# Optimization experiments

Hardware: AMD Instinct MI355X
Metric: run time of the kernel (lower is better)

The kernel has to match this reference:

```python
import jax, jax.numpy as jnp
import numpy as np

B, L, H, NH, HD, DI, NL = 8, 4096, 256, 4, 64, 1024, 6
_SCALE = 1.0 / np.sqrt(HD).astype(np.float32)


def _layernorm(x, g, b, eps=1e-5):
    m = x.mean(-1, keepdims=True)
    v = ((x - m) ** 2).mean(-1, keepdims=True)
    return (x - m) / jnp.sqrt(v + eps) * g + b


def _forward(data, mask, pos_emb, ln_g, ln_b, ff_w1, ff_b1, ff_w2, ff_b2,
             ff_lng, ff_lnb, ring_wq, ring_bq, ring_wk, ring_bk, ring_wv,
             ring_bv, ring_wo, ring_bo, star_wq, star_bq, star_wk, star_bk,
             star_wv, star_bv, star_wo, star_bo):
    pad = ~mask                                         # [B,L] True = padding
    spad = jnp.concatenate([jnp.zeros((B, 1), bool), pad], axis=1)  # [B,L+1]
    x = data + pos_emb[None, :L]                        # [B,L,H] (emb dropout = eval identity)
    nodes = x
    relay = x.mean(axis=1)                              # [B,H]
    for i in range(NL):
        # --- PositionwiseFeedForward (1x1 conv == dense over channels) ---
        h = nodes
        t = jax.nn.relu(h @ ff_w1[i].T + ff_b1[i]) @ ff_w2[i].T + ff_b2[i]
        h = _layernorm(t + h, ff_lng[i], ff_lnb[i])     # [B,L,H]
        # --- ring attention (_MSA1): size-3 sliding window + global relay key ---
        q = (h @ ring_wq[i].T + ring_bq[i]).reshape(B, L, NH, HD)
        k = (h @ ring_wk[i].T + ring_bk[i]).reshape(B, L, NH, HD)
        v = (h @ ring_wv[i].T + ring_bv[i]).reshape(B, L, NH, HD)
        kp = jnp.pad(k, ((0, 0), (1, 1), (0, 0), (0, 0)))  # zero pad, matches F.unfold
        vp = jnp.pad(v, ((0, 0), (1, 1), (0, 0), (0, 0)))
        k_win = jnp.stack([kp[:, 0:L], kp[:, 1:L + 1], kp[:, 2:L + 2]], axis=2)  # [B,L,3,NH,HD]
        v_win = jnp.stack([vp[:, 0:L], vp[:, 1:L + 1], vp[:, 2:L + 2]], axis=2)
        ak = (relay @ ring_wk[i].T + ring_bk[i]).reshape(B, 1, 1, NH, HD)
        av = (relay @ ring_wv[i].T + ring_bv[i]).reshape(B, 1, 1, NH, HD)
        k_all = jnp.concatenate([k_win, jnp.broadcast_to(ak, (B, L, 1, NH, HD))], axis=2)
        v_all = jnp.concatenate([v_win, jnp.broadcast_to(av, (B, L, 1, NH, HD))], axis=2)
        scores = jnp.einsum('blnd,blwnd->blwn', q, k_all) * _SCALE
        alphas = jax.nn.softmax(scores, axis=2)         # softmax over window dim (4)
        att = jnp.einsum('blwn,blwnd->blnd', alphas, v_all).reshape(B, L, NH * HD)
        ring_out = att @ ring_wo[i].T + ring_bo[i]
        nodes = jax.nn.leaky_relu(_layernorm(ring_out, ln_g[i], ln_b[i]))
        # --- star attention (_MSA2): relay attends to [relay; nodes] ---
        y = jnp.concatenate([relay[:, None, :], nodes], axis=1)  # [B,L+1,H]
        sq = (relay @ star_wq[i].T + star_bq[i]).reshape(B, NH, HD)
        sk = (y @ star_wk[i].T + star_bk[i]).reshape(B, L + 1, NH, HD)
        sv = (y @ star_wv[i].T + star_bv[i]).reshape(B, L + 1, NH, HD)
        s = jnp.einsum('bnd,blnd->bnl', sq, sk) * _SCALE
        s = jnp.where(spad[:, None, :], -jnp.inf, s)
        a = jax.nn.softmax(s, axis=-1)
        satt = jnp.einsum('bnl,blnd->bnd', a, sv).reshape(B, NH * HD)
        relay = jax.nn.leaky_relu(satt @ star_wo[i].T + star_bo[i])
        nodes = jnp.where(pad[:, :, None], 0.0, nodes)
    return nodes, relay


def setup_inputs() -> dict:
    key = jax.random.key(0)
    ks = iter(jax.random.split(key, 64))
    p = lambda shape: jax.random.normal(next(ks), shape, jnp.float32) * 0.02
    C = NH * HD
    return dict(
        data=jax.random.normal(next(ks), (B, L, H), jnp.float32),
        mask=jnp.ones((B, L), bool),
        pos_emb=p((L, H)),
        ln_g=jnp.ones((NL, H), jnp.float32), ln_b=jnp.zeros((NL, H), jnp.float32),
        ff_w1=p((NL, DI, H)), ff_b1=jnp.zeros((NL, DI), jnp.float32),
        ff_w2=p((NL, H, DI)), ff_b2=jnp.zeros((NL, H), jnp.float32),
        ff_lng=jnp.ones((NL, H), jnp.float32), ff_lnb=jnp.zeros((NL, H), jnp.float32),
        ring_wq=p((NL, C, H)), ring_bq=jnp.zeros((NL, C), jnp.float32),
        ring_wk=p((NL, C, H)), ring_bk=jnp.zeros((NL, C), jnp.float32),
        ring_wv=p((NL, C, H)), ring_bv=jnp.zeros((NL, C), jnp.float32),
        ring_wo=p((NL, H, C)), ring_bo=jnp.zeros((NL, H), jnp.float32),
        star_wq=p((NL, C, H)), star_bq=jnp.zeros((NL, C), jnp.float32),
        star_wk=p((NL, C, H)), star_bk=jnp.zeros((NL, C), jnp.float32),
        star_wv=p((NL, C, H)), star_bv=jnp.zeros((NL, C), jnp.float32),
        star_wo=p((NL, H, C)), star_bo=jnp.zeros((NL, H), jnp.float32),
    )


def reference(data, mask, pos_emb, ln_g, ln_b, ff_w1, ff_b1, ff_w2, ff_b2,
              ff_lng, ff_lnb, ring_wq, ring_bq, ring_wk, ring_bk, ring_wv,
              ring_bv, ring_wo, ring_bo, star_wq, star_bq, star_wk, star_bk,
              star_wv, star_bv, star_wo, star_bo):
    return _forward(data, mask, pos_emb, ln_g, ln_b, ff_w1, ff_b1, ff_w2,
                    ff_b2, ff_lng, ff_lnb, ring_wq, ring_bq, ring_wk, ring_bk,
                    ring_wv, ring_bv, ring_wo, ring_bo, star_wq, star_bq,
                    star_wk, star_bk, star_wv, star_bv, star_wo, star_bo)
```

## Files before the change

### kernel.cpp

```cpp
#include <hip/hip_runtime.h>
#include <hip/hip_bf16.h>

#define B_ 8
#define L_ 4096
#define H_ 256
#define NH_ 4
#define DI_ 1024
#define NL_ 6
#define TOK_ (B_*L_)

typedef unsigned short u16;
typedef __attribute__((ext_vector_type(8))) short short8;
typedef __attribute__((ext_vector_type(4))) float f32x4;

struct __align__(8) u16x4 { u16 x,y,z,w; };

__device__ __forceinline__ float bf2f(u16 u){
  union { unsigned u; float f; } c; c.u = ((unsigned)u)<<16; return c.f;
}
__device__ __forceinline__ u16 f2bf(float f){
  union { float f; unsigned u; } c; c.f = f;
  unsigned r = c.u + 0x7FFF + ((c.u>>16)&1);
  return (u16)(r>>16);
}
__device__ __forceinline__ void gload_lds16(const short* g, short* l){
  __builtin_amdgcn_global_load_lds(
      (const __attribute__((address_space(1))) void*)g,
      (__attribute__((address_space(3))) void*)l, 16, 0, 0);
}
__device__ __forceinline__ void block_sync(){
  asm volatile("" ::: "memory");
  __builtin_amdgcn_s_barrier();
  __builtin_amdgcn_sched_barrier(0);
}
#define WAIT_VMCNT(N) asm volatile("s_waitcnt vmcnt(" #N ")" ::: "memory")

template<bool RELU, bool OBF16>
__global__ __launch_bounds__(512, 4) void gemm_bt(
    const u16* __restrict__ A, const u16* __restrict__ W,
    const float* __restrict__ bias, void* __restrict__ out, int N, int K, int nbn)
{
  constexpr int BM=128, BK=64;
  __shared__ __align__(16) short As[2][BM*BK];
  __shared__ __align__(16) short Ws[2][BM*BK];
  const int tid = threadIdx.x, lane = tid&63, wid = tid>>6;
  const int wm = wid>>1, wn = wid&1;
  const int id = blockIdx.x;
  const int xcd = id & 7, j = id >> 3;
  const int bm = xcd*32 + j / nbn;
  const int bn = j % nbn;
  const short* Ag = (const short*)A + (size_t)bm*BM*K;
  const short* Wg = (const short*)W + (size_t)bn*BM*K;
  f32x4 acc[2][4] = {};

  auto STAGE = [&](int k0, int buf){
    #pragma unroll
    for (int jj=0;jj<2;++jj){
      int c = jj*512 + tid;
      int row = c>>3;
      int col = (c&7) ^ (row&7);
      const size_t src = (size_t)row*K + k0 + col*8;
      gload_lds16(Ag + src, &As[buf][(size_t)c*8]);
      gload_lds16(Wg + src, &Ws[buf][(size_t)c*8]);
    }
  };
  auto COMPUTE = [&](int cur){
    #pragma unroll
    for (int kk=0;kk<BK;kk+=32){
      short8 af[2], bfr[4];
      int kc = (kk>>3) + (lane>>4);
      #pragma unroll
      for (int ms=0;ms<2;++ms){
        int r = wm*32 + ms*16 + (lane&15);
        af[ms] = *(const short8*)&As[cur][r*BK + ((kc ^ (r&7))<<3)];
      }
      #pragma unroll
      for (int ns=0;ns<4;++ns){
        int r = wn*64 + ns*16 + (lane&15);
        bfr[ns] = *(const short8*)&Ws[cur][r*BK + ((kc ^ (r&7))<<3)];
      }
      #pragma unroll
      for (int ms=0;ms<2;++ms)
        #pragma unroll
        for (int ns=0;ns<4;++ns)
          acc[ms][ns] = __builtin_amdgcn_mfma_f32_16x16x32_bf16(af[ms], bfr[ns], acc[ms][ns], 0, 0, 0);
    }
  };

  const int NT = K/BK;
  STAGE(0, 0); STAGE(BK, 1);
  WAIT_VMCNT(4);
  block_sync();
  for (int t=0;t<NT;++t){
    const int cur = t&1;
    __builtin_amdgcn_s_setprio(1);
    COMPUTE(cur);
    __builtin_amdgcn_s_setprio(0);
    block_sync();
    if (t+2 < NT) STAGE((t+2)*BK, cur);
    if (t+1 < NT){
      if (t+2 < NT) { WAIT_VMCNT(4); }
      else          { WAIT_VMCNT(0); }
      block_sync();
    }
  }
  if (OBF16){
    constexpr int OP = 136;
    u16* O = (u16*)&As[0][0];
    #pragma unroll
    for (int ns=0;ns<4;++ns){
      int lc = wn*64 + ns*16 + (lane&15);
      float bc = bias[bn*BM + lc];
      #pragma unroll
      for (int ms=0;ms<2;++ms){
        int rbase = wm*32 + ms*16 + ((lane>>4)<<2);
        #pragma unroll
        for (int i=0;i<4;++i){
          float v = acc[ms][ns][i] + bc;
          if (RELU) v = fmaxf(v, 0.f);
          O[(rbase+i)*OP + lc] = f2bf(v);
        }
      }
    }
    block_sync();
    u16* ob = (u16*)out + (size_t)bm*BM*N + bn*BM;
    const int rr = tid>>4;
    const int cc = (tid&15)<<3;
    #pragma unroll
    for (int p=0;p<4;++p){
      int r = p*32 + rr;
      *reinterpret_cast<short8*>(ob + (size_t)r*N + cc) =
          *reinterpret_cast<const short8*>(&O[r*OP + cc]);
    }
  } else {
    const int r0 = bm*BM + wm*32;
    const int c0 = bn*BM + wn*64;
    #pragma unroll
    for (int ns=0;ns<4;++ns){
      int col = c0 + ns*16 + (lane&15);
      float bc = bias[col];
      #pragma unroll
      for (int ms=0;ms<2;++ms){
        int rbase = r0 + ms*16 + ((lane>>4)<<2);
        #pragma unroll
        for (int i=0;i<4;++i){
          float v = acc[ms][ns][i] + bc;
          if (RELU) v = fmaxf(v, 0.f);
          ((float*)out)[(size_t)(rbase+i)*N + col] = v;
        }
      }
    }
  }
}

template<bool ADDRES, bool LEAKY>
__global__ __launch_bounds__(512, 4) void gemm_ln(
    const u16* __restrict__ A, const u16* __restrict__ W,
    const float* __restrict__ bias, const u16* __restrict__ res,
    const float* __restrict__ g, const float* __restrict__ bv,
    u16* __restrict__ outb, float* __restrict__ outf, int K)
{
  constexpr int BM=64, BK=64;
  __shared__ __align__(16) short As[2][BM*BK];
  __shared__ __align__(16) short Ws[2][256*BK];
  float* S1  = (float*)&As[0][0];
  float* S2  = S1 + 64*4;
  float* MU  = S2 + 64*4;
  float* RSD = MU + 64;
  const int tid = threadIdx.x, lane = tid&63, wid = tid>>6;
  const int wm = wid>>2, wn = wid&3;
  const int m0 = blockIdx.x*BM;
  const short* Ag = (const short*)A + (size_t)m0*K;
  const short* Wg = (const short*)W;
  f32x4 acc[2][4] = {};

  auto STAGE = [&](int k0, int buf){
    {
      int c = tid;
      int row = c>>3;
      int col = (c&7) ^ (row&7);
      gload_lds16(Ag + (size_t)row*K + k0 + col*8, &As[buf][(size_t)c*8]);
    }
    #pragma unroll
    for (int jj=0;jj<4;++jj){
      int c = jj*512 + tid;
      int row = c>>3;
      int col = (c&7) ^ (row&7);
      gload_lds16(Wg + (size_t)row*K + k0 + col*8, &Ws[buf][(size_t)c*8]);
    }
  };
  auto COMPUTE = [&](int cur){
    #pragma unroll
    for (int kk=0;kk<BK;kk+=32){
      short8 af[2], bfr[4];
      int kc = (kk>>3) + (lane>>4);
      #pragma unroll
      for (int ms=0;ms<2;++ms){
        int r = wm*32 + ms*16 + (lane&15);
        af[ms] = *(const short8*)&As[cur][r*BK + ((kc ^ (r&7))<<3)];
      }
      #pragma unroll
      for (int ns=0;ns<4;++ns){
        int r = wn*64 + ns*16 + (lane&15);
        bfr[ns] = *(const short8*)&Ws[cur][r*BK + ((kc ^ (r&7))<<3)];
      }
      #pragma unroll
      for (int ms=0;ms<2;++ms)
        #pragma unroll
        for (int ns=0;ns<4;++ns)
          acc[ms][ns] = __builtin_amdgcn_mfma_f32_16x16x32_bf16(af[ms], bfr[ns], acc[ms][ns], 0, 0, 0);
    }
  };

  const int NT = K/BK;
  STAGE(0, 0); STAGE(BK, 1);
  WAIT_VMCNT(5);
  block_sync();
  for (int t=0;t<NT;++t){
    const int cur = t&1;
    __builtin_amdgcn_s_setprio(1);
    COMPUTE(cur);
    __builtin_amdgcn_s_setprio(0);
    block_sync();
    if (t+2 < NT) STAGE((t+2)*BK, cur);
    if (t+1 < NT){
      if (t+2 < NT) { WAIT_VMCNT(5); }
      else          { WAIT_VMCNT(0); }
      block_sync();
    }
  }
  #pragma unroll
  for (int ns=0;ns<4;++ns){
    int col = wn*64 + ns*16 + (lane&15);
    float bc = bias[col];
    #pragma unroll
    for (int ms=0;ms<2;++ms){
      int rl = wm*32 + ms*16 + ((lane>>4)<<2);
      #pragma unroll
      for (int i=0;i<4;++i){
        float v = acc[ms][ns][i] + bc;
        if (ADDRES) v += bf2f(res[(size_t)(m0+rl+i)*256 + col]);
        acc[ms][ns][i] = v;
      }
    }
  }
  #pragma unroll
  for (int ms=0;ms<2;++ms)
    #pragma unroll
    for (int i=0;i<4;++i){
      float p1 = acc[ms][0][i]+acc[ms][1][i]+acc[ms][2][i]+acc[ms][3][i];
      float p2 = acc[ms][0][i]*acc[ms][0][i] + acc[ms][1][i]*acc[ms][1][i]
               + acc[ms][2][i]*acc[ms][2][i] + acc[ms][3][i]*acc[ms][3][i];
      #pragma unroll
      for (int o=1;o<16;o<<=1){ p1 += __shfl_xor(p1,o,64); p2 += __shfl_xor(p2,o,64); }
      if ((lane&15)==0){
        int rl = wm*32 + ms*16 + ((lane>>4)<<2) + i;
        S1[rl*4 + wn] = p1; S2[rl*4 + wn] = p2;
      }
    }
  __syncthreads();
  if (tid < 64){
    float s1 = S1[tid*4+0]+S1[tid*4+1]+S1[tid*4+2]+S1[tid*4+3];
    float s2 = S2[tid*4+0]+S2[tid*4+1]+S2[tid*4+2]+S2[tid*4+3];
    float mean = s1*(1.f/256.f);
    float var = fmaxf(s2*(1.f/256.f) - mean*mean, 0.f);
    MU[tid] = mean; RSD[tid] = 1.f/sqrtf(var + 1e-5f);
  }
  __syncthreads();
  constexpr int OP = 268;
  u16* O = (u16*)&Ws[0][0];
  #pragma unroll
  for (int ns=0;ns<4;++ns){
    int col = wn*64 + ns*16 + (lane&15);
    float gg = g[col], bb = bv[col];
    #pragma unroll
    for (int ms=0;ms<2;++ms){
      int rl = wm*32 + ms*16 + ((lane>>4)<<2);
      #pragma unroll
      for (int i=0;i<4;++i){
        float y = (acc[ms][ns][i] - MU[rl+i])*RSD[rl+i]*gg + bb;
        if (LEAKY) y = y>0.f ? y : 0.01f*y;
        O[(rl+i)*OP + col] = f2bf(y);
        if (outf) outf[(size_t)(m0+rl+i)*256 + col] = y;
      }
    }
  }
  __syncthreads();
  u16* ob = outb + (size_t)m0*256;
  const int rr = tid>>5;
  const int cc = (tid&31)<<3;
  #pragma unroll
  for (int p=0;p<4;++p){
    int r = p*16 + rr;
    *reinterpret_cast<short8*>(ob + ((size_t)r<<8) + cc) =
        *reinterpret_cast<const short8*>(&O[r*OP + cc]);
  }
}

__global__ __launch_bounds__(256) void ring_attn(
    const u16* __restrict__ qkv, const float* __restrict__ akav, u16* __restrict__ att)
{
  const int g = blockIdx.x*4 + (threadIdx.x>>6);
  const int lane = threadIdx.x & 63;
  const int l = g & (L_-1);
  const int b = g >> 12;
  const size_t tok = (size_t)g;
  float q[4], kp[4], kc[4], kn[4], ak[4], vp[4], vc[4], vn[4], av[4];
  {
    u16x4 t = *(const u16x4*)(qkv + tok*768 + lane*4);
    q[0]=bf2f(t.x); q[1]=bf2f(t.y); q[2]=bf2f(t.z); q[3]=bf2f(t.w);
    t = *(const u16x4*)(qkv + tok*768 + 256 + lane*4);
    kc[0]=bf2f(t.x); kc[1]=bf2f(t.y); kc[2]=bf2f(t.z); kc[3]=bf2f(t.w);
    t = *(const u16x4*)(qkv + tok*768 + 512 + lane*4);
    vc[0]=bf2f(t.x); vc[1]=bf2f(t.y); vc[2]=bf2f(t.z); vc[3]=bf2f(t.w);
    if (l>0){
      t = *(const u16x4*)(qkv + (tok-1)*768 + 256 + lane*4);
      kp[0]=bf2f(t.x); kp[1]=bf2f(t.y); kp[2]=bf2f(t.z); kp[3]=bf2f(t.w);
      t = *(const u16x4*)(qkv + (tok-1)*768 + 512 + lane*4);
      vp[0]=bf2f(t.x); vp[1]=bf2f(t.y); vp[2]=bf2f(t.z); vp[3]=bf2f(t.w);
    } else { kp[0]=kp[1]=kp[2]=kp[3]=0.f; vp[0]=vp[1]=vp[2]=vp[3]=0.f; }
    if (l<L_-1){
      t = *(const u16x4*)(qkv + (tok+1)*768 + 256 + lane*4);
      kn[0]=bf2f(t.x); kn[1]=bf2f(t.y); kn[2]=bf2f(t.z); kn[3]=bf2f(t.w);
      t = *(const u16x4*)(qkv + (tok+1)*768 + 512 + lane*4);
      vn[0]=bf2f(t.x); vn[1]=bf2f(t.y); vn[2]=bf2f(t.z); vn[3]=bf2f(t.w);
    } else { kn[0]=kn[1]=kn[2]=kn[3]=0.f; vn[0]=vn[1]=vn[2]=vn[3]=0.f; }
    float4 f = ((const float4*)(akav + (size_t)b*H_))[lane];
    ak[0]=f.x; ak[1]=f.y; ak[2]=f.z; ak[3]=f.w;
    f = ((const float4*)(akav + 2048 + (size_t)b*H_))[lane];
    av[0]=f.x; av[1]=f.y; av[2]=f.z; av[3]=f.w;
  }
  float dp=0.f, dc=0.f, dn=0.f, da=0.f;
  #pragma unroll
  for (int j=0;j<4;++j){ dp += q[j]*kp[j]; dc += q[j]*kc[j]; dn += q[j]*kn[j]; da += q[j]*ak[j]; }
  #pragma unroll
  for (int o=1;o<16;o<<=1){
    dp += __shfl_xor(dp,o,64); dc += __shfl_xor(dc,o,64);
    dn += __shfl_xor(dn,o,64); da += __shfl_xor(da,o,64);
  }
  dp *= 0.125f; dc *= 0.125f; dn *= 0.125f; da *= 0.125f;
  float m = fmaxf(fmaxf(dp,dc), fmaxf(dn,da));
  float e0 = expf(dp-m), e1 = expf(dc-m), e2 = expf(dn-m), e3 = expf(da-m);
  float rd = 1.f/(e0+e1+e2+e3);
  u16x4 o4;
  o4.x = f2bf((e0*vp[0]+e1*vc[0]+e2*vn[0]+e3*av[0])*rd);
  o4.y = f2bf((e0*vp[1]+e1*vc[1]+e2*vn[1]+e3*av[1])*rd);
  o4.z = f2bf((e0*vp[2]+e1*vc[2]+e2*vn[2]+e3*av[2])*rd);
  o4.w = f2bf((e0*vp[3]+e1*vc[3]+e2*vn[3]+e3*av[3])*rd);
  *(u16x4*)(att + tok*H_ + lane*4) = o4;
}

__global__ __launch_bounds__(256) void star_scores(
    const u16* __restrict__ skv, const float* __restrict__ sq,
    const float* __restrict__ sk0, float* __restrict__ s)
{
  const int g = blockIdx.x*4 + (threadIdx.x>>6);
  if (g >= B_*(L_+1)) return;
  const int lane = threadIdx.x & 63;
  const int b = g/(L_+1), j = g%(L_+1);
  float4 qv = ((const float4*)(sq + (size_t)b*H_))[lane];
  float k0,k1,k2,k3;
  if (j==0){
    float4 kv = ((const float4*)(sk0 + (size_t)b*H_))[lane];
    k0=kv.x; k1=kv.y; k2=kv.z; k3=kv.w;
  } else {
    u16x4 t = *(const u16x4*)(skv + ((size_t)b*L_ + (j-1))*512 + lane*4);
    k0=bf2f(t.x); k1=bf2f(t.y); k2=bf2f(t.z); k3=bf2f(t.w);
  }
  float d = qv.x*k0 + qv.y*k1 + qv.z*k2 + qv.w*k3;
  #pragma unroll
  for (int o=1;o<16;o<<=1) d += __shfl_xor(d,o,64);
  if ((lane&15)==0)
    s[(size_t)(b*4 + (lane>>4))*(L_+1) + j] = d*0.125f;
}

__global__ __launch_bounds__(1024) void star_softmax(float* __restrict__ s)
{
  const int bh = blockIdx.x;
  float* row = s + (size_t)bh*(L_+1);
  __shared__ float red[1024];
  const int tid = threadIdx.x;
  float m = -1e30f;
  for (int j=tid; j<L_+1; j+=1024) m = fmaxf(m, row[j]);
  red[tid] = m; __syncthreads();
  for (int st=512; st>0; st>>=1){ if (tid<st) red[tid] = fmaxf(red[tid], red[tid+st]); __syncthreads(); }
  m = red[0]; __syncthreads();
  float sum = 0.f;
  for (int j=tid; j<L_+1; j+=1024){ float e = expf(row[j]-m); row[j] = e; sum += e; }
  red[tid] = sum; __syncthreads();
  for (int st=512; st>0; st>>=1){ if (tid<st) red[tid] += red[tid+st]; __syncthreads(); }
  const float rs = 1.f/red[0];
  for (int j=tid; j<L_+1; j+=1024) row[j] *= rs;
}

__global__ __launch_bounds__(256) void star_satt_part(
    const float* __restrict__ a, const u16* __restrict__ skv, float* __restrict__ part)
{
  const int blk = blockIdx.x;
  const int b = blk >> 6, seg = blk & 63;
  const int tid = threadIdx.x, q4 = tid & 63, sub = tid >> 6;
  const int h = q4 >> 4;
  const float* arow = a + (size_t)(b*4 + h)*(L_+1) + 1;
  float a0=0.f,a1=0.f,a2=0.f,a3=0.f;
  const int j0 = seg*64 + sub*16;
  #pragma unroll 4
  for (int jj=j0; jj<j0+16; ++jj){
    u16x4 v = *(const u16x4*)(skv + ((size_t)b*L_ + jj)*512 + 256 + q4*4);
    float al = arow[jj];
    a0 += al*bf2f(v.x); a1 += al*bf2f(v.y); a2 += al*bf2f(v.z); a3 += al*bf2f(v.w);
  }
  __shared__ float red[4][256];
  red[sub][q4*4+0]=a0; red[sub][q4*4+1]=a1; red[sub][q4*4+2]=a2; red[sub][q4*4+3]=a3;
  __syncthreads();
  if (sub==0){
    #pragma unroll
    for (int c=0;c<4;++c){
      int ch = q4*4+c;
      part[(size_t)blk*256 + ch] = red[0][ch]+red[1][ch]+red[2][ch]+red[3][ch];
    }
  }
}

__global__ __launch_bounds__(256) void pack_wT(
    const float* __restrict__ w0, const float* __restrict__ w1,
    const float* __restrict__ w2, const float* __restrict__ w3,
    const float* __restrict__ w4, const float* __restrict__ w5,
    float* __restrict__ T)
{
  __shared__ float tile[32][33];
  const int blk = blockIdx.x;
  const int t = blk & 63, m = blk >> 6;
  const int l = m / 6, w = m % 6;
  const float* srcs[6] = {w0, w1, w2, w3, w4, w5};
  const float* src = srcs[w] + (size_t)l*65536;
  const int r0 = (t>>3)*32, c0 = (t&7)*32;
  const int rr = threadIdx.x >> 5, cc = threadIdx.x & 31;
  #pragma unroll
  for (int p=0;p<4;++p)
    tile[rr + p*8][cc] = src[(size_t)(r0 + rr + p*8)*256 + c0 + cc];
  __syncthreads();
  float* dst = T + (size_t)m*65536;
  #pragma unroll
  for (int p=0;p<4;++p)
    dst[(size_t)(c0 + rr + p*8)*256 + r0 + cc] = tile[cc][rr + p*8];
}

struct TPB { const float* b; float* out; };
struct TPB5 { TPB p[5]; };
__global__ __launch_bounds__(256) void relay_projs(
    const float* __restrict__ relay, const float* __restrict__ TW, TPB5 tp)
{
  const int b = blockIdx.x, w = blockIdx.y, n = threadIdx.x;
  __shared__ float rs[H_];
  rs[n] = relay[b*H_ + n];
  __syncthreads();
  const float* wt = TW + (size_t)w*65536;
  float s = tp.p[w].b[n];
  #pragma unroll 8
  for (int c=0;c<H_;++c) s += rs[c]*wt[(size_t)c*256 + n];
  tp.p[w].out[b*H_+n] = s;
}

__global__ __launch_bounds__(256) void relay_tail_k(
    const float* __restrict__ part, const float* __restrict__ a,
    const float* __restrict__ sv0, const float* __restrict__ TW,
    const float* __restrict__ bo, float* __restrict__ relay, float* __restrict__ outr)
{
  const int b = blockIdx.x, n = threadIdx.x;
  __shared__ float rs[H_];
  const int h = n >> 6;
  float s = a[(size_t)(b*4+h)*(L_+1)] * sv0[b*H_ + n];
  #pragma unroll 8
  for (int g2=0; g2<64; ++g2) s += part[((size_t)b*64+g2)*256 + n];
  rs[n] = s;
  __syncthreads();
  const float* wt = TW + (size_t)5*65536;
  float v = bo[n];
  #pragma unroll 8
  for (int c=0;c<H_;++c) v += rs[c]*wt[(size_t)c*256 + n];
  v = v>0.f ? v : 0.01f*v;
  relay[b*H_+n] = v;
  if (outr) outr[b*H_+n] = v;
}

__global__ void f32_to_bf16_k(const float* __restrict__ s, u16* __restrict__ d, int n){
  for (int i = blockIdx.x*blockDim.x + threadIdx.x; i < n; i += gridDim.x*blockDim.x)
    d[i] = f2bf(s[i]);
}
__global__ void pack_wqkv(const float* __restrict__ wq, const float* __restrict__ wk,
                          const float* __restrict__ wv, u16* __restrict__ dst){
  const int n = NL_*768*H_;
  for (int i = blockIdx.x*blockDim.x + threadIdx.x; i < n; i += gridDim.x*blockDim.x){
    int l = i/(768*H_); int rem = i%(768*H_); int r = rem/H_; int c = rem%H_;
    float v = (r<256) ? wq[((size_t)l*H_ + r)*H_ + c]
            : (r<512) ? wk[((size_t)l*H_ + (r-256))*H_ + c]
                      : wv[((size_t)l*H_ + (r-512))*H_ + c];
    dst[i] = f2bf(v);
  }
}
__global__ void pack_wskv(const float* __restrict__ wk, const float* __restrict__ wv, u16* __restrict__ dst){
  const int n = NL_*512*H_;
  for (int i = blockIdx.x*blockDim.x + threadIdx.x; i < n; i += gridDim.x*blockDim.x){
    int l = i/(512*H_); int rem = i%(512*H_); int r = rem/H_; int c = rem%H_;
    float v = (r<256) ? wk[((size_t)l*H_ + r)*H_ + c]
                      : wv[((size_t)l*H_ + (r-256))*H_ + c];
    dst[i] = f2bf(v);
  }
}
__global__ void pack_biases(const float* __restrict__ bq, const float* __restrict__ bk,
                            const float* __restrict__ bv, float* __restrict__ dqkv,
                            const float* __restrict__ sbk, const float* __restrict__ sbv,
                            float* __restrict__ dskv){
  int i = blockIdx.x*blockDim.x + threadIdx.x;
  if (i < NL_*768){
    int l = i/768, r = i%768;
    dqkv[i] = (r<256) ? bq[l*H_+r] : (r<512) ? bk[l*H_+r-256] : bv[l*H_+r-512];
  }
  if (i < NL_*512){
    int l = i/512, r = i%512;
    dskv[i] = (r<256) ? sbk[l*H_+r] : sbv[l*H_+r-256];
  }
}
__global__ void init_nodes(const float* __restrict__ data, const float* __restrict__ pos, u16* __restrict__ nodes){
  const int total = TOK_*H_/4;
  int i = blockIdx.x*blockDim.x + threadIdx.x;
  if (i >= total) return;
  float4 d = ((const float4*)data)[i];
  float4 p = ((const float4*)pos)[i % (L_*H_/4)];
  u16x4 o; o.x=f2bf(d.x+p.x); o.y=f2bf(d.y+p.y); o.z=f2bf(d.z+p.z); o.w=f2bf(d.w+p.w);
  ((u16x4*)nodes)[i] = o;
}
__global__ void relay_partial(const float* __restrict__ data, const float* __restrict__ pos, float* __restrict__ part){
  const int b = blockIdx.x>>3, seg = blockIdx.x&7, hh = threadIdx.x;
  float s = 0.f;
  for (int l = seg*512; l < seg*512+512; ++l)
    s += data[((size_t)b*L_ + l)*H_ + hh] + pos[(size_t)l*H_ + hh];
  part[blockIdx.x*H_ + hh] = s;
}
__global__ void relay_combine(const float* __restrict__ part, float* __restrict__ relay){
  const int b = blockIdx.x, hh = threadIdx.x;
  float s = 0.f;
  for (int g=0; g<8; ++g) s += part[(b*8+g)*H_ + hh];
  relay[b*H_+hh] = s * (1.0f/L_);
}

extern "C" void kernel_launch(void* const* d_in, const int* in_sizes, int n_in,
                              void* d_out, int out_size, void* d_ws, size_t ws_size,
                              hipStream_t stream)
{
  const float* data   = (const float*)d_in[0];
  const float* pos    = (const float*)d_in[2];
  const float* ln_g   = (const float*)d_in[3];
  const float* ln_b   = (const float*)d_in[4];
  const float* ff_w1  = (const float*)d_in[5];
  const float* ff_b1  = (const float*)d_in[6];
  const float* ff_w2  = (const float*)d_in[7];
  const float* ff_b2  = (const float*)d_in[8];
  const float* ff_lng = (const float*)d_in[9];
  const float* ff_lnb = (const float*)d_in[10];
  const float* ring_wq= (const float*)d_in[11]; const float* ring_bq= (const float*)d_in[12];
  const float* ring_wk= (const float*)d_in[13]; const float* ring_bk= (const float*)d_in[14];
  const float* ring_wv= (const float*)d_in[15]; const float* ring_bv= (const float*)d_in[16];
  const float* ring_wo= (const float*)d_in[17]; const float* ring_bo= (const float*)d_in[18];
  const float* star_wq= (const float*)d_in[19]; const float* star_bq= (const float*)d_in[20];
  const float* star_wk= (const float*)d_in[21]; const float* star_bk= (const float*)d_in[22];
  const float* star_wv= (const float*)d_in[23]; const float* star_bv= (const float*)d_in[24];
  const float* star_wo= (const float*)d_in[25]; const float* star_bo= (const float*)d_in[26];

  char* ws = (char*)d_ws;
  size_t off = 0;
  auto alc = [&](size_t n){ size_t cur = off; off = (cur + n + 255) & ~(size_t)255; return (void*)(ws + cur); };
  u16*  W1B   = (u16*)alc((size_t)NL_*DI_*H_*2);
  u16*  W2B   = (u16*)alc((size_t)NL_*H_*DI_*2);
  u16*  WQKVB = (u16*)alc((size_t)NL_*768*H_*2);
  u16*  WOB   = (u16*)alc((size_t)NL_*H_*H_*2);
  u16*  WSKVB = (u16*)alc((size_t)NL_*512*H_*2);
  float* BQKVB= (float*)alc((size_t)NL_*768*4);
  float* BSKVB= (float*)alc((size_t)NL_*512*4);
  float* TWB  = (float*)alc((size_t)NL_*6*H_*H_*4);
  u16*  NB    = (u16*)alc((size_t)TOK_*H_*2);
  u16*  HB    = (u16*)alc((size_t)TOK_*H_*2);
  u16*  T1R   = (u16*)alc((size_t)TOK_*DI_*2);
  float* RELAY  = (float*)alc(B_*H_*4);
  float* PART   = (float*)alc(64*H_*4);
  float* AKAV   = (float*)alc(2*B_*H_*4);
  float* SQB    = (float*)alc(B_*H_*4);
  float* SK0B   = (float*)alc(B_*H_*4);
  float* SV0B   = (float*)alc(B_*H_*4);
  float* SBUF   = (float*)alc((size_t)B_*NH_*(L_+1)*4);
  float* SPART  = (float*)alc((size_t)B_*64*256*4);
  u16* QKVB = T1R;
  u16* ATTB = T1R + (size_t)TOK_*768;
  u16* SKVB = T1R;

  f32_to_bf16_k<<<2048, 256, 0, stream>>>(ff_w1, W1B, NL_*DI_*H_);
  f32_to_bf16_k<<<2048, 256, 0, stream>>>(ff_w2, W2B, NL_*H_*DI_);
  f32_to_bf16_k<<<1024, 256, 0, stream>>>(ring_wo, WOB, NL_*H_*H_);
  pack_wqkv<<<2048, 256, 0, stream>>>(ring_wq, ring_wk, ring_wv, WQKVB);
  pack_wskv<<<2048, 256, 0, stream>>>(star_wk, star_wv, WSKVB);
  pack_biases<<<18, 256, 0, stream>>>(ring_bq, ring_bk, ring_bv, BQKVB, star_bk, star_bv, BSKVB);
  pack_wT<<<NL_*6*64, 256, 0, stream>>>(ring_wk, ring_wv, star_wq, star_wk, star_wv, star_wo, TWB);

  init_nodes<<<(TOK_*H_/4 + 255)/256, 256, 0, stream>>>(data, pos, NB);
  relay_partial<<<64, 256, 0, stream>>>(data, pos, PART);
  relay_combine<<<B_, 256, 0, stream>>>(PART, RELAY);

  for (int l=0; l<NL_; ++l){
    const float* TWl = TWB + (size_t)l*6*H_*H_;
    gemm_bt<true,true><<<(DI_/128)*(TOK_/128), 512, 0, stream>>>(
        NB, W1B + (size_t)l*DI_*H_, ff_b1 + l*DI_, T1R, DI_, H_, DI_/128);
    gemm_ln<true,false><<<TOK_/64, 512, 0, stream>>>(
        T1R, W2B + (size_t)l*H_*DI_, ff_b2 + l*H_, NB,
        ff_lng + l*H_, ff_lnb + l*H_, HB, nullptr, DI_);
    TPB5 tp;
    tp.p[0] = { ring_bk + l*H_, AKAV };
    tp.p[1] = { ring_bv + l*H_, AKAV + 2048 };
    tp.p[2] = { star_bq + l*H_, SQB };
    tp.p[3] = { star_bk + l*H_, SK0B };
    tp.p[4] = { star_bv + l*H_, SV0B };
    relay_projs<<<dim3(B_,5), 256, 0, stream>>>(RELAY, TWl, tp);
    gemm_bt<false,true><<<(768/128)*(TOK_/128), 512, 0, stream>>>(
        HB, WQKVB + (size_t)l*768*H_, BQKVB + l*768, QKVB, 768, H_, 768/128);
    ring_attn<<<TOK_/4, 256, 0, stream>>>(QKVB, AKAV, ATTB);
    gemm_ln<false,true><<<TOK_/64, 512, 0, stream>>>(
        ATTB, WOB + (size_t)l*H_*H_, ring_bo + l*H_, nullptr,
        ln_g + l*H_, ln_b + l*H_, NB,
        (l==NL_-1) ? (float*)d_out : nullptr, H_);
    gemm_bt<false,true><<<(512/128)*(TOK_/128), 512, 0, stream>>>(
        NB, WSKVB + (size_t)l*512*H_, BSKVB + l*512, SKVB, 512, H_, 512/128);
    star_scores<<<(B_*(L_+1) + 3)/4, 256, 0, stream>>>(SKVB, SQB, SK0B, SBUF);
    star_softmax<<<B_*NH_, 1024, 0, stream>>>(SBUF);
    star_satt_part<<<B_*64, 256, 0, stream>>>(SBUF, SKVB, SPART);
    relay_tail_k<<<B_, 256, 0, stream>>>(SPART, SBUF, SV0B, TWl,
        star_bo + l*H_, RELAY,
        (l==NL_-1) ? ((float*)d_out + (size_t)TOK_*H_) : nullptr);
  }
}
```

Measured before the change: 1.097 ms.

## Fuse ring attention into output-projection GEMM with LayerNorm epilogue

Replaces the separate ring_attn kernel and the following gemm_ln with a single attn_ln kernel. Each 64-row block computes the windowed attention output directly into a swizzled LDS A tile, then runs the Wo GEMM while streaming W in double-buffered chunks, and applies bias, LayerNorm and leaky ReLU in the epilogue. This removes one launch and the global write and re-read of the attention tensor. In exchange it uses much more LDS per block, which may lower occupancy, and the attention loads are serialised ahead of the GEMM.

Measured after the change: 1.072 ms. 1.02x faster.

```diff
diff --git a/kernel.cpp b/kernel.cpp
--- a/kernel.cpp
+++ b/kernel.cpp
@@ -34,6 +34,7 @@
   __builtin_amdgcn_sched_barrier(0);
 }
 #define WAIT_VMCNT(N) asm volatile("s_waitcnt vmcnt(" #N ")" ::: "memory")
+#define WAIT_LGKM0()  asm volatile("s_waitcnt lgkmcnt(0)" ::: "memory")
 
 template<bool RELU, bool OBF16>
 __global__ __launch_bounds__(512, 4) void gemm_bt(
@@ -297,57 +298,186 @@
   }
 }
 
-__global__ __launch_bounds__(256) void ring_attn(
-    const u16* __restrict__ qkv, const float* __restrict__ akav, u16* __restrict__ att)
-{
-  const int g = blockIdx.x*4 + (threadIdx.x>>6);
-  const int lane = threadIdx.x & 63;
-  const int l = g & (L_-1);
-  const int b = g >> 12;
-  const size_t tok = (size_t)g;
-  float q[4], kp[4], kc[4], kn[4], ak[4], vp[4], vc[4], vn[4], av[4];
-  {
-    u16x4 t = *(const u16x4*)(qkv + tok*768 + lane*4);
-    q[0]=bf2f(t.x); q[1]=bf2f(t.y); q[2]=bf2f(t.z); q[3]=bf2f(t.w);
-    t = *(const u16x4*)(qkv + tok*768 + 256 + lane*4);
-    kc[0]=bf2f(t.x); kc[1]=bf2f(t.y); kc[2]=bf2f(t.z); kc[3]=bf2f(t.w);
-    t = *(const u16x4*)(qkv + tok*768 + 512 + lane*4);
-    vc[0]=bf2f(t.x); vc[1]=bf2f(t.y); vc[2]=bf2f(t.z); vc[3]=bf2f(t.w);
+__global__ __launch_bounds__(512, 4) void attn_ln(
+    const u16* __restrict__ qkv, const float* __restrict__ akav,
+    const u16* __restrict__ W, const float* __restrict__ bo,
+    const float* __restrict__ g, const float* __restrict__ bv,
+    u16* __restrict__ outb, float* __restrict__ outf)
+{
+  constexpr int BK=32, NT=256/BK;
+  __shared__ __align__(16) char LB[74240];
+  short* Afull = (short*)LB;
+  short* Ws2   = (short*)(LB + 32768);
+  float* S1  = (float*)(LB + 65536);
+  float* S2  = S1 + 256;
+  float* MU  = S2 + 256;
+  float* RSD = MU + 64;
+  const int tid = threadIdx.x, lane = tid&63, wid = tid>>6;
+  const int wm = wid>>2, wn = wid&3;
+  const int m0 = blockIdx.x*64;
+  const short* Wg = (const short*)W;
+
+  auto STAGE_W = [&](int k0, int buf){
+    #pragma unroll
+    for (int jj=0;jj<2;++jj){
+      int c = jj*512 + tid;
+      int row = c>>2;
+      int col = (c&3) ^ (row&3);
+      gload_lds16(Wg + (size_t)row*256 + k0 + col*8, &Ws2[(size_t)buf*8192 + (size_t)c*8]);
+    }
+  };
+
+  STAGE_W(0, 0); STAGE_W(BK, 1);
+  __builtin_amdgcn_sched_barrier(0);
+
+  for (int it=0; it<8; ++it){
+    const int rl = wid*8 + it;
+    const size_t tok = (size_t)(m0 + rl);
+    const int l = (int)(tok & (L_-1));
+    const int b = (int)(tok >> 12);
+    float q[4], kp[4], kc[4], kn[4], ak[4], vp[4], vc[4], vn[4], av[4];
+    u16x4 t4 = *(const u16x4*)(qkv + tok*768 + lane*4);
+    q[0]=bf2f(t4.x); q[1]=bf2f(t4.y); q[2]=bf2f(t4.z); q[3]=bf2f(t4.w);
+    t4 = *(const u16x4*)(qkv + tok*768 + 256 + lane*4);
+    kc[0]=bf2f(t4.x); kc[1]=bf2f(t4.y); kc[2]=bf2f(t4.z); kc[3]=bf2f(t4.w);
+    t4 = *(const u16x4*)(qkv + tok*768 + 512 + lane*4);
+    vc[0]=bf2f(t4.x); vc[1]=bf2f(t4.y); vc[2]=bf2f(t4.z); vc[3]=bf2f(t4.w);
     if (l>0){
-      t = *(const u16x4*)(qkv + (tok-1)*768 + 256 + lane*4);
-      kp[0]=bf2f(t.x); kp[1]=bf2f(t.y); kp[2]=bf2f(t.z); kp[3]=bf2f(t.w);
-      t = *(const u16x4*)(qkv + (tok-1)*768 + 512 + lane*4);
-      vp[0]=bf2f(t.x); vp[1]=bf2f(t.y); vp[2]=bf2f(t.z); vp[3]=bf2f(t.w);
+      t4 = *(const u16x4*)(qkv + (tok-1)*768 + 256 + lane*4);
+      kp[0]=bf2f(t4.x); kp[1]=bf2f(t4.y); kp[2]=bf2f(t4.z); kp[3]=bf2f(t4.w);
+      t4 = *(const u16x4*)(qkv + (tok-1)*768 + 512 + lane*4);
+      vp[0]=bf2f(t4.x); vp[1]=bf2f(t4.y); vp[2]=bf2f(t4.z); vp[3]=bf2f(t4.w);
     } else { kp[0]=kp[1]=kp[2]=kp[3]=0.f; vp[0]=vp[1]=vp[2]=vp[3]=0.f; }
     if (l<L_-1){
-      t = *(const u16x4*)(qkv + (tok+1)*768 + 256 + lane*4);
-      kn[0]=bf2f(t.x); kn[1]=bf2f(t.y); kn[2]=bf2f(t.z); kn[3]=bf2f(t.w);
-      t = *(const u16x4*)(qkv + (tok+1)*768 + 512 + lane*4);
-      vn[0]=bf2f(t.x); vn[1]=bf2f(t.y); vn[2]=bf2f(t.z); vn[3]=bf2f(t.w);
+      t4 = *(const u16x4*)(qkv + (tok+1)*768 + 256 + lane*4);
+      kn[0]=bf2f(t4.x); kn[1]=bf2f(t4.y); kn[2]=bf2f(t4.z); kn[3]=bf2f(t4.w);
+      t4 = *(const u16x4*)(qkv + (tok+1)*768 + 512 + lane*4);
+      vn[0]=bf2f(t4.x); vn[1]=bf2f(t4.y); vn[2]=bf2f(t4.z); vn[3]=bf2f(t4.w);
     } else { kn[0]=kn[1]=kn[2]=kn[3]=0.f; vn[0]=vn[1]=vn[2]=vn[3]=0.f; }
-    float4 f = ((const float4*)(akav + (size_t)b*H_))[lane];
-    ak[0]=f.x; ak[1]=f.y; ak[2]=f.z; ak[3]=f.w;
-    f = ((const float4*)(akav + 2048 + (size_t)b*H_))[lane];
-    av[0]=f.x; av[1]=f.y; av[2]=f.z; av[3]=f.w;
-  }
-  float dp=0.f, dc=0.f, dn=0.f, da=0.f;
-  #pragma unroll
-  for (int j=0;j<4;++j){ dp += q[j]*kp[j]; dc += q[j]*kc[j]; dn += q[j]*kn[j]; da += q[j]*ak[j]; }
-  #pragma unroll
-  for (int o=1;o<16;o<<=1){
-    dp += __shfl_xor(dp,o,64); dc += __shfl_xor(dc,o,64);
-    dn += __shfl_xor(dn,o,64); da += __shfl_xor(da,o,64);
-  }
-  dp *= 0.125f; dc *= 0.125f; dn *= 0.125f; da *= 0.125f;
-  float m = fmaxf(fmaxf(dp,dc), fmaxf(dn,da));
-  float e0 = expf(dp-m), e1 = expf(dc-m), e2 = expf(dn-m), e3 = expf(da-m);
-  float rd = 1.f/(e0+e1+e2+e3);
-  u16x4 o4;
-  o4.x = f2bf((e0*vp[0]+e1*vc[0]+e2*vn[0]+e3*av[0])*rd);
-  o4.y = f2bf((e0*vp[1]+e1*vc[1]+e2*vn[1]+e3*av[1])*rd);
-  o4.z = f2bf((e0*vp[2]+e1*vc[2]+e2*vn[2]+e3*av[2])*rd);
-  o4.w = f2bf((e0*vp[3]+e1*vc[3]+e2*vn[3]+e3*av[3])*rd);
-  *(u16x4*)(att + tok*H_ + lane*4) = o4;
+    float4 f4 = ((const float4*)(akav + (size_t)b*H_))[lane];
+    ak[0]=f4.x; ak[1]=f4.y; ak[2]=f4.z; ak[3]=f4.w;
+    f4 = ((const float4*)(akav + 2048 + (size_t)b*H_))[lane];
+    av[0]=f4.x; av[1]=f4.y; av[2]=f4.z; av[3]=f4.w;
+    float dp=0.f, dc=0.f, dn=0.f, da=0.f;
+    #pragma unroll
+    for (int jc=0;jc<4;++jc){ dp += q[jc]*kp[jc]; dc += q[jc]*kc[jc]; dn += q[jc]*kn[jc]; da += q[jc]*ak[jc]; }
+    #pragma unroll
+    for (int o=1;o<16;o<<=1){
+      dp += __shfl_xor(dp,o,64); dc += __shfl_xor(dc,o,64);
+      dn += __shfl_xor(dn,o,64); da += __shfl_xor(da,o,64);
+    }
+    dp *= 0.125f; dc *= 0.125f; dn *= 0.125f; da *= 0.125f;
+    float m = fmaxf(fmaxf(dp,dc), fmaxf(dn,da));
+    float e0 = expf(dp-m), e1 = expf(dc-m), e2 = expf(dn-m), e3 = expf(da-m);
+    float rd = 1.f/(e0+e1+e2+e3);
+    u16x4 o4;
+    o4.x = f2bf((e0*vp[0]+e1*vc[0]+e2*vn[0]+e3*av[0])*rd);
+    o4.y = f2bf((e0*vp[1]+e1*vc[1]+e2*vn[1]+e3*av[1])*rd);
+    o4.z = f2bf((e0*vp[2]+e1*vc[2]+e2*vn[2]+e3*av[2])*rd);
+    o4.w = f2bf((e0*vp[3]+e1*vc[3]+e2*vn[3]+e3*av[3])*rd);
+    int gq = lane>>1;
+    int s = (gq & ~7) | ((gq&7) ^ (rl&7));
+    *(u16x4*)&Afull[rl*256 + s*8 + (lane&1)*4] = o4;
+  }
+  WAIT_LGKM0();
+  WAIT_VMCNT(2);
+  block_sync();
+
+  f32x4 acc[2][4] = {};
+  for (int t=0;t<NT;++t){
+    const int cur = t&1;
+    __builtin_amdgcn_s_setprio(1);
+    {
+      short8 af[2], bfr[4];
+      #pragma unroll
+      for (int ms=0;ms<2;++ms){
+        int r = wm*32 + ms*16 + (lane&15);
+        int gk = t*4 + (lane>>4);
+        int s = (gk & ~7) | ((gk&7) ^ (r&7));
+        af[ms] = *(const short8*)&Afull[r*256 + s*8];
+      }
+      #pragma unroll
+      for (int ns=0;ns<4;++ns){
+        int r2 = wn*64 + ns*16 + (lane&15);
+        int sl = (lane>>4) ^ (r2&3);
+        bfr[ns] = *(const short8*)&Ws2[(size_t)cur*8192 + r2*32 + sl*8];
+      }
+      #pragma unroll
+      for (int ms=0;ms<2;++ms)
+        #pragma unroll
+        for (int ns=0;ns<4;++ns)
+          acc[ms][ns] = __builtin_amdgcn_mfma_f32_16x16x32_bf16(af[ms], bfr[ns], acc[ms][ns], 0, 0, 0);
+    }
+    __builtin_amdgcn_s_setprio(0);
+    block_sync();
+    if (t+2 < NT) STAGE_W((t+2)*BK, cur);
+    if (t+1 < NT){
+      if (t+2 < NT) { WAIT_VMCNT(2); }
+      else          { WAIT_VMCNT(0); }
+      block_sync();
+    }
+  }
+
+  #pragma unroll
+  for (int ns=0;ns<4;++ns){
+    int col = wn*64 + ns*16 + (lane&15);
+    float bc = bo[col];
+    #pragma unroll
+    for (int ms=0;ms<2;++ms)
+      #pragma unroll
+      for (int i=0;i<4;++i)
+        acc[ms][ns][i] += bc;
+  }
+  #pragma unroll
+  for (int ms=0;ms<2;++ms)
+    #pragma unroll
+    for (int i=0;i<4;++i){
+      float p1 = acc[ms][0][i]+acc[ms][1][i]+acc[ms][2][i]+acc[ms][3][i];
+      float p2 = acc[ms][0][i]*acc[ms][0][i] + acc[ms][1][i]*acc[ms][1][i]
+               + acc[ms][2][i]*acc[ms][2][i] + acc[ms][3][i]*acc[ms][3][i];
+      #pragma unroll
+      for (int o=1;o<16;o<<=1){ p1 += __shfl_xor(p1,o,64); p2 += __shfl_xor(p2,o,64); }
+      if ((lane&15)==0){
+        int rl = wm*32 + ms*16 + ((lane>>4)<<2) + i;
+        S1[rl*4 + wn] = p1; S2[rl*4 + wn] = p2;
+      }
+    }
+  __syncthreads();
+  if (tid < 64){
+    float s1 = S1[tid*4+0]+S1[tid*4+1]+S1[tid*4+2]+S1[tid*4+3];
+    float s2 = S2[tid*4+0]+S2[tid*4+1]+S2[tid*4+2]+S2[tid*4+3];
+    float mean = s1*(1.f/256.f);
+    float var = fmaxf(s2*(1.f/256.f) - mean*mean, 0.f);
+    MU[tid] = mean; RSD[tid] = 1.f/sqrtf(var + 1e-5f);
+  }
+  __syncthreads();
+  constexpr int OP = 268;
+  u16* O = (u16*)LB;
+  #pragma unroll
+  for (int ns=0;ns<4;++ns){
+    int col = wn*64 + ns*16 + (lane&15);
+    float gg = g[col], bb = bv[col];
+    #pragma unroll
+    for (int ms=0;ms<2;++ms){
+      int rl = wm*32 + ms*16 + ((lane>>4)<<2);
+      #pragma unroll
+      for (int i=0;i<4;++i){
+        float y = (acc[ms][ns][i] - MU[rl+i])*RSD[rl+i]*gg + bb;
+        y = y>0.f ? y : 0.01f*y;
+        O[(rl+i)*OP + col] = f2bf(y);
+        if (outf) outf[(size_t)(m0+rl+i)*256 + col] = y;
+      }
+    }
+  }
+  __syncthreads();
+  u16* ob = outb + (size_t)m0*256;
+  const int rr = tid>>5, cc = (tid&31)<<3;
+  #pragma unroll
+  for (int p=0;p<4;++p){
+    int r = p*16 + rr;
+    *reinterpret_cast<short8*>(ob + ((size_t)r<<8) + cc) =
+        *reinterpret_cast<const short8*>(&O[r*OP + cc]);
+  }
 }
 
 __global__ __launch_bounds__(256) void star_scores(
@@ -590,7 +720,6 @@
   float* SBUF   = (float*)alc((size_t)B_*NH_*(L_+1)*4);
   float* SPART  = (float*)alc((size_t)B_*64*256*4);
   u16* QKVB = T1R;
-  u16* ATTB = T1R + (size_t)TOK_*768;
   u16* SKVB = T1R;
 
   f32_to_bf16_k<<<2048, 256, 0, stream>>>(ff_w1, W1B, NL_*DI_*H_);
@@ -621,11 +750,10 @@
     relay_projs<<<dim3(B_,5), 256, 0, stream>>>(RELAY, TWl, tp);
     gemm_bt<false,true><<<(768/128)*(TOK_/128), 512, 0, stream>>>(
         HB, WQKVB + (size_t)l*768*H_, BQKVB + l*768, QKVB, 768, H_, 768/128);
-    ring_attn<<<TOK_/4, 256, 0, stream>>>(QKVB, AKAV, ATTB);
-    gemm_ln<false,true><<<TOK_/64, 512, 0, stream>>>(
-        ATTB, WOB + (size_t)l*H_*H_, ring_bo + l*H_, nullptr,
+    attn_ln<<<TOK_/64, 512, 0, stream>>>(
+        QKVB, AKAV, WOB + (size_t)l*H_*H_, ring_bo + l*H_,
         ln_g + l*H_, ln_b + l*H_, NB,
-        (l==NL_-1) ? (float*)d_out : nullptr, H_);
+        (l==NL_-1) ? (float*)d_out : nullptr);
     gemm_bt<false,true><<<(512/128)*(TOK_/128), 512, 0, stream>>>(
         NB, WSKVB + (size_t)l*512*H_, BSKVB + l*512, SKVB, 512, H_, 512/128);
     star_scores<<<(B_*(L_+1) + 3)/4, 256, 0, stream>>>(SKVB, SQB, SK0B, SBUF);
```
